# Kernel tuning notes

Measured on AMD Instinct MI355X. Metric: run time of the kernel, lower is better.

Reference implementation:

```python
import jax, jax.numpy as jnp
import numpy as np

B, L, D = 4, 4096, 1024  # batch, seq, d_model == in_features == out_features
E, R = 8, 8              # n_experts, r_base
DH = D // 2              # router hidden


def setup_inputs() -> dict:
    key = jax.random.key(0)
    ks = jax.random.split(key, 8)
    s = 0.02
    return {
        "x": jax.random.normal(ks[0], (B, L, D), dtype=jnp.float32),
        "W_base": jax.random.normal(ks[1], (D, D), dtype=jnp.float32) * s,
        "router_W1": jax.random.normal(ks[2], (DH, D), dtype=jnp.float32) * s,
        "router_b1": jnp.zeros((DH,), dtype=jnp.float32),
        "router_W2": jax.random.normal(ks[3], (E, DH), dtype=jnp.float32) * s,
        "router_b2": jnp.zeros((E,), dtype=jnp.float32),
        "temperature": jnp.asarray(1.0, dtype=jnp.float32),
        "lora_A": jax.random.normal(ks[4], (E, R, D), dtype=jnp.float32) * s,
        "lora_B": jax.random.normal(ks[5], (E, D, R), dtype=jnp.float32) * s,
    }


def reference(x, W_base, router_W1, router_b1, router_W2, router_b2,
              temperature, lora_A, lora_B):
    # Base frozen linear (bias=False): [B,L,D]
    base = jnp.einsum("bld,od->blo", x, W_base)
    # Router (eval mode: dropout inactive). hidden_states = x (Identity projection).
    h = jax.nn.relu(jnp.einsum("bld,hd->blh", x, router_W1) + router_b1)
    logits = (jnp.einsum("blh,eh->ble", h, router_W2) + router_b2) / temperature
    gates = jax.nn.softmax(logits, axis=-1)  # softmax over experts, [B,L,E]
    # All experts' low-rank projections batched: x @ A_e.T -> [B,L,E,R]
    xa = jnp.einsum("bld,erd->bler", x, lora_A)
    # Gate-weighted up-projection and sum over experts: [B,L,D]
    lora_out = jnp.einsum("bler,ble,edr->bld", xa, gates, lora_B)
    return base + lora_out
```

## Files before the change

### kernel.cpp

```cpp
#include <hip/hip_runtime.h>
#include <hip/hip_bf16.h>
#include <stdint.h>
#include <math.h>


#define M_TOK 16384

typedef unsigned short u16;
typedef short bf16x8 __attribute__((ext_vector_type(8)));
typedef float f32x4 __attribute__((ext_vector_type(4)));
typedef __attribute__((address_space(3))) uint32_t lds_u32_t;
typedef __attribute__((address_space(1))) const uint32_t glb_u32_t;

__device__ __forceinline__ u16 f2bf(float f) {
  uint32_t u = __builtin_bit_cast(uint32_t, f);
  return (u16)((u + 0x7fffu + ((u >> 16) & 1u)) >> 16);
}
__device__ __forceinline__ float bf2f(u16 v) {
  return __builtin_bit_cast(float, (uint32_t)v << 16);
}

#define VMCNT(n) asm volatile("s_waitcnt vmcnt(%0)" ::"i"(n) : "memory")
#define BAR asm volatile("s_barrier" ::: "memory")
#define SP(x) __builtin_amdgcn_s_setprio(x)

__global__ __launch_bounds__(256) void prep_k(const float* __restrict__ x,
                                              const float* __restrict__ Wb,
                                              const float* __restrict__ rW1,
                                              const float* __restrict__ rW2,
                                              const float* __restrict__ loraA,
                                              const float* __restrict__ loraB,
                                              u16* __restrict__ xb,
                                              u16* __restrict__ Btb,
                                              u16* __restrict__ W1b,
                                              u16* __restrict__ W2b,
                                              u16* __restrict__ A2b) {
  const int g = blockIdx.x;
  const int tid = threadIdx.x;
  if (g < 16384) {
    int i = g * 256 + tid;
    float4 v = ((const float4*)x)[i];
    ushort4 o;
    o.x = f2bf(v.x); o.y = f2bf(v.y); o.z = f2bf(v.z); o.w = f2bf(v.w);
    ((ushort4*)xb)[i] = o;
  } else if (g < 17408) {
    int i = (g - 16384) * 256 + tid;
    int idx = i * 4;
    int row = idx >> 10, col = idx & 1023;
    float4 v = ((const float4*)Wb)[i];
    ushort4 o;
    o.x = f2bf(v.x); o.y = f2bf(v.y); o.z = f2bf(v.z); o.w = f2bf(v.w);
    *(ushort4*)(Btb + (size_t)row * 1088 + col) = o;
  } else if (g < 17920) {
    int i = (g - 17408) * 256 + tid;
    float4 v = ((const float4*)rW1)[i];
    ushort4 o;
    o.x = f2bf(v.x); o.y = f2bf(v.y); o.z = f2bf(v.z); o.w = f2bf(v.w);
    ((ushort4*)W1b)[i] = o;
  } else if (g < 18176) {
    int idx = (g - 17920) * 256 + tid;
    int n = idx >> 6, q = idx & 63;
    int e = q >> 3, r = q & 7;
    Btb[(size_t)n * 1088 + 1024 + q] = f2bf(loraB[((size_t)(e * 1024 + n)) * 8 + r]);
  } else if (g < 18240) {
    int i = (g - 18176) * 256 + tid;
    float4 v = ((const float4*)loraA)[i];
    ushort4 o;
    o.x = f2bf(v.x); o.y = f2bf(v.y); o.z = f2bf(v.z); o.w = f2bf(v.w);
    ((ushort4*)A2b)[i] = o;
  } else {
    int i = (g - 18240) * 256 + tid;
    int idx = i * 4;
    int row = idx >> 9, col = idx & 511;
    ushort4 o = {0, 0, 0, 0};
    if (row < 8) {
      float4 v = *(const float4*)(rW2 + (size_t)row * 512 + col);
      o.x = f2bf(v.x); o.y = f2bf(v.y); o.z = f2bf(v.z); o.w = f2bf(v.w);
    }
    ((ushort4*)W2b)[i] = o;
  }
}

__global__ __launch_bounds__(256) void gemm_w(const u16* __restrict__ A,
                                              const u16* __restrict__ Bt,
                                              const float* __restrict__ part,
                                              const float* __restrict__ b2,
                                              const float* __restrict__ temp,
                                              u16* __restrict__ Cv) {
  constexpr int BM = 64, BN = 64, FM = 2, FN = 2, AI = 2, BI = 2;
  __shared__ u16 lds[(BM + BN) * 64];
  __shared__ float g_lds[64][8];
  u16* As = lds;
  u16* Bs = lds + BM * 64;

  const int tid = threadIdx.x;
  const int w = tid >> 6, lane = tid & 63;
  const int wr = w >> 1, wc = w & 1;
  const int m0 = blockIdx.y * BM;

  if (tid < 64) {
    const int m = m0 + tid;
    float lg[8] = {};
#pragma unroll
    for (int q = 0; q < 4; ++q) {
      const float4* pp = (const float4*)(part + ((size_t)q * M_TOK + m) * 8);
      float4 a = pp[0], b = pp[1];
      lg[0] += a.x; lg[1] += a.y; lg[2] += a.z; lg[3] += a.w;
      lg[4] += b.x; lg[5] += b.y; lg[6] += b.z; lg[7] += b.w;
    }
    float t = temp[0], mx = -1e30f;
#pragma unroll
    for (int e = 0; e < 8; ++e) { lg[e] = (lg[e] + b2[e]) / t; mx = fmaxf(mx, lg[e]); }
    float s = 0.f;
#pragma unroll
    for (int e = 0; e < 8; ++e) { lg[e] = expf(lg[e] - mx); s += lg[e]; }
    float inv = 1.f / s;
#pragma unroll
    for (int e = 0; e < 8; ++e) g_lds[tid][e] = lg[e] * inv;
  }

  const uint8_t* Ab = (const uint8_t*)A;
  const uint8_t* Bb = (const uint8_t*)Bt;
  f32x4 acc[FM][FN] = {};

  for (int kt = 0; kt < 16; ++kt) {
#pragma unroll
    for (int i = 0; i < AI; ++i) {
      const int lbase = (w * AI + i) * 1024;
      const int o = lbase + lane * 16;
      const int r = o >> 7, cb = o & 127;
      const uint8_t* g = Ab + (size_t)(m0 + r) * 2048 + (size_t)kt * 128 + cb;
      __builtin_amdgcn_global_load_lds((glb_u32_t*)g,
                                       (lds_u32_t*)((uint8_t*)As + lbase), 16, 0, 0);
    }
#pragma unroll
    for (int i = 0; i < BI; ++i) {
      const int lbase = (w * BI + i) * 1024;
      const int o = lbase + lane * 16;
      const int r = o >> 7, cb = o & 127;
      const uint8_t* g = Bb + (size_t)r * 2048 + (size_t)kt * 128 + cb;
      __builtin_amdgcn_global_load_lds((glb_u32_t*)g,
                                       (lds_u32_t*)((uint8_t*)Bs + lbase), 16, 0, 0);
    }
    __syncthreads();

    bf16x8 af[2][FM], bfv[2][FN];
#pragma unroll
    for (int ks = 0; ks < 2; ++ks) {
      const int col = ks * 32 + ((lane >> 4) << 3);
#pragma unroll
      for (int im = 0; im < FM; ++im) {
        const int row = wr * 32 + im * 16 + (lane & 15);
        af[ks][im] = *(const bf16x8*)(As + row * 64 + col);
      }
#pragma unroll
      for (int in_ = 0; in_ < FN; ++in_) {
        const int row = wc * 32 + in_ * 16 + (lane & 15);
        bfv[ks][in_] = *(const bf16x8*)(Bs + row * 64 + col);
      }
    }
#pragma unroll
    for (int ks = 0; ks < 2; ++ks)
#pragma unroll
      for (int im = 0; im < FM; ++im)
#pragma unroll
        for (int in_ = 0; in_ < FN; ++in_)
          acc[im][in_] = __builtin_amdgcn_mfma_f32_16x16x32_bf16(
              af[ks][im], bfv[ks][in_], acc[im][in_], 0, 0, 0);
    __syncthreads();
  }

#pragma unroll
  for (int im = 0; im < FM; ++im)
#pragma unroll
    for (int in_ = 0; in_ < FN; ++in_) {
      const int col = wc * 32 + in_ * 16 + (lane & 15);
#pragma unroll
      for (int j = 0; j < 4; ++j) {
        const int lrow = wr * 32 + im * 16 + ((lane >> 4) << 2) + j;
        float v = acc[im][in_][j] * g_lds[lrow][col >> 3];
        Cv[(size_t)(m0 + lrow) * 64 + col] = f2bf(v);
      }
    }
}

__global__ __launch_bounds__(512, 2) void gemm_h(const u16* __restrict__ A,
                                                 const u16* __restrict__ Bt,
                                                 const u16* __restrict__ W2bv,
                                                 float* __restrict__ part,
                                                 const float* __restrict__ aux,
                                                 const int N, const int K,
                                                 const int lda, const int ldb) {
  constexpr int BM = 256, BN = 128, FMH = 4;
  constexpr int BUFB = (BM + BN) * 128;

  __shared__ __align__(16) uint8_t lds[2 * BUFB];

  const int tid = threadIdx.x;
  const int lane = tid & 63, w = tid >> 6;
  const int wr = w >> 2, wcn = w & 3;
  const int l15 = lane & 15, lhi = lane >> 4;
  const int xorv = (lane & 7) << 4;
  const int c0 = (lhi * 16) ^ xorv;
  const int c1 = (64 + lhi * 16) ^ xorv;

  const int f = blockIdx.x;
  const int idx = (f & 7) * 32 + (f >> 3);
  const int gx = N / BN;
  const int m0 = (idx / gx) * BM;
  const int n0 = (idx % gx) * BN;

  const size_t lda_b = (size_t)lda * 2, ldb_b = (size_t)ldb * 2;
  const int nk = K >> 6;
  const int arow0 = (wr * (BM / 2) + l15) * 128;
  const int brow0 = (wcn * (BN / 4) + l15) * 128;

  f32x4 acc[8][2] = {};
  bf16x8 A0f[FMH][2], A1f[FMH][2];
  bf16x8 Bf[2][2];

  auto stageA = [&](int h, int kt, int b) {
    const int ktc = kt < nk ? kt : nk - 1;
    uint8_t* dst = lds + b * BUFB + h * (BM * 64) + w * 1024;
#pragma unroll
    for (int i = 0; i < 2; ++i) {
      const int off = i * 8192 + tid * 16;
      const int row = h * (BM / 2) + (off >> 7);
      const int ss = ((off >> 4) & 7) ^ (row & 7);
      const uint8_t* g =
          (const uint8_t*)A + (size_t)(m0 + row) * lda_b + ktc * 128 + ss * 16;
      __builtin_amdgcn_global_load_lds((glb_u32_t*)g, (lds_u32_t*)(dst + i * 8192),
                                       16, 0, 0);
    }
  };
  auto stageB = [&](int kt, int b) {
    const int ktc = kt < nk ? kt : nk - 1;
    uint8_t* dst = lds + b * BUFB + BM * 128 + w * 1024;
#pragma unroll
    for (int i = 0; i < 2; ++i) {
      const int off = i * 8192 + tid * 16;
      const int row = off >> 7;
      const int ss = ((off >> 4) & 7) ^ (row & 7);
      const uint8_t* g =
          (const uint8_t*)Bt + (size_t)(n0 + row) * ldb_b + ktc * 128 + ss * 16;
      __builtin_amdgcn_global_load_lds((glb_u32_t*)g, (lds_u32_t*)(dst + i * 8192),
                                       16, 0, 0);
    }
  };
  auto loadA = [&](int mh, const uint8_t* buf, bf16x8 (&dst)[FMH][2]) {
#pragma unroll
    for (int im2 = 0; im2 < FMH; ++im2) {
      const uint8_t* p = buf + arow0 + mh * (FMH * 2048) + im2 * 2048;
      dst[im2][0] = *(const bf16x8*)(p + c0);
      dst[im2][1] = *(const bf16x8*)(p + c1);
    }
  };
  auto loadB = [&](const uint8_t* buf) {
#pragma unroll
    for (int nh = 0; nh < 2; ++nh) {
      const uint8_t* p = buf + BM * 128 + brow0 + nh * 2048;
      Bf[nh][0] = *(const bf16x8*)(p + c0);
      Bf[nh][1] = *(const bf16x8*)(p + c1);
    }
  };

#define H_MFMA(mh, AF)                                                         \
  _Pragma("unroll") for (int im2 = 0; im2 < FMH; ++im2)                        \
  _Pragma("unroll") for (int nh = 0; nh < 2; ++nh)                             \
  _Pragma("unroll") for (int ks = 0; ks < 2; ++ks)                             \
      acc[(mh) * FMH + im2][nh] = __builtin_amdgcn_mfma_f32_16x16x32_bf16(     \
          AF[im2][ks], Bf[nh][ks], acc[(mh) * FMH + im2][nh], 0, 0, 0);

  stageB(0, 0);
  stageA(0, 0, 0); stageA(1, 0, 0);
  stageB(1, 1);

#pragma unroll 1
  for (int t = 0; t < nk; ++t) {
    const int p = t & 1, q = p ^ 1;
    const uint8_t* bp = (const uint8_t*)lds + p * BUFB;
    stageA(0, t + 1, q); stageA(1, t + 1, q);
    VMCNT(6);
    BAR;
    loadB(bp);
    loadA(0, bp, A0f);
    SP(1); H_MFMA(0, A0f); SP(0);
    loadA(1, bp, A1f);
    BAR;
    stageB(t + 2, p);
    BAR;
    SP(1); H_MFMA(1, A1f); SP(0);
    BAR;
  }

  u16* hs = (u16*)lds;
  __syncthreads();
#pragma unroll
  for (int im = 0; im < 8; ++im) {
#pragma unroll
    for (int in_ = 0; in_ < 2; ++in_) {
      const int col = wcn * 32 + in_ * 16 + l15;
#pragma unroll
      for (int j = 0; j < 4; ++j) {
        const int row = wr * 128 + im * 16 + lhi * 4 + j;
        float v = fmaxf(acc[im][in_][j] + aux[n0 + col], 0.f);
        hs[row * 132 + col] = f2bf(v);
      }
    }
  }
  __syncthreads();
  const u16* w2b = W2bv;
  f32x4 acc2[2] = {};
#pragma unroll
  for (int ks = 0; ks < 4; ++ks) {
    bf16x8 bfrag = *(const bf16x8*)(w2b + (size_t)l15 * 512 + n0 + ks * 32 + lhi * 8);
#pragma unroll
    for (int im2 = 0; im2 < 2; ++im2) {
      const int mrow = w * 32 + im2 * 16 + l15;
      bf16x8 afrag = *(const bf16x8*)(hs + mrow * 132 + ks * 32 + lhi * 8);
      acc2[im2] = __builtin_amdgcn_mfma_f32_16x16x32_bf16(afrag, bfrag, acc2[im2],
                                                          0, 0, 0);
    }
  }
  if (l15 < 8) {
    const size_t base = (size_t)(n0 >> 7) * M_TOK;
#pragma unroll
    for (int im2 = 0; im2 < 2; ++im2)
#pragma unroll
      for (int j = 0; j < 4; ++j) {
        const int row = m0 + w * 32 + im2 * 16 + lhi * 4 + j;
        part[(base + row) * 8 + l15] = acc2[im2][j];
      }
  }
}

#define MFMA_Q2(mh, nh, AF, BF)                                                \
  _Pragma("unroll") for (int im2 = 0; im2 < 4; ++im2)                          \
  _Pragma("unroll") for (int in2 = 0; in2 < 2; ++in2)                          \
  _Pragma("unroll") for (int ks = 0; ks < 2; ++ks)                             \
      acc[(mh) * 4 + im2][(nh) * 2 + in2] =                                    \
          __builtin_amdgcn_mfma_f32_16x16x32_bf16(                             \
              AF[im2][ks], BF[in2][ks],                                        \
              acc[(mh) * 4 + im2][(nh) * 2 + in2], 0, 0, 0);

__global__ __launch_bounds__(512, 2) void gemm_out(const u16* __restrict__ A,
                                                   const u16* __restrict__ Bt,
                                                   const u16* __restrict__ A2,
                                                   float* __restrict__ C,
                                                   const int N, const int K,
                                                   const int lda, const int ldb) {
  constexpr int BM = 256, BN = 256;
  constexpr int VMC = 4;
  constexpr int BUFB = (BM + BN) * 128;

  __shared__ __align__(16) uint8_t lds[2 * BUFB];

  const int tid = threadIdx.x;
  const int lane = tid & 63, w = tid >> 6;
  const int wr = w >> 2, wcn = w & 3;
  const int l15 = lane & 15, lhi = lane >> 4;
  const int xorv = (lane & 7) << 4;
  const int c0 = (lhi * 16) ^ xorv;
  const int c1 = (64 + lhi * 16) ^ xorv;

  const int f = blockIdx.x;
  const int idx = (f & 7) * 32 + (f >> 3);
  const int gx = N / BN;
  const int m0 = (idx / gx) * BM;
  const int n0 = (idx % gx) * BN;

  const size_t lda_b = (size_t)lda * 2, ldb_b = (size_t)ldb * 2;
  const int nk = K >> 6;
  const int arow0 = (wr * (BM / 2) + l15) * 128;
  const int brow0 = (wcn * (BN / 4) + l15) * 128;

  f32x4 acc[8][4] = {};
  bf16x8 A0f[4][2], A1f[4][2];
  bf16x8 B0f[2][2], B1f[2][2];

  auto stageA = [&](int h, int kt, int b) {
    const int ktc = kt < nk ? kt : nk - 1;
    const bool last = (ktc == nk - 1);
    uint8_t* dst = lds + b * BUFB + h * (BM * 64) + w * 1024;
#pragma unroll
    for (int i = 0; i < 2; ++i) {
      const int off = i * 8192 + tid * 16;
      const int row = h * (BM / 2) + (off >> 7);
      const int ss = ((off >> 4) & 7) ^ (row & 7);
      const uint8_t* g =
          last ? (const uint8_t*)A2 + (size_t)(m0 + row) * 128 + ss * 16
               : (const uint8_t*)A + (size_t)(m0 + row) * lda_b + ktc * 128 + ss * 16;
      __builtin_amdgcn_global_load_lds((glb_u32_t*)g, (lds_u32_t*)(dst + i * 8192),
                                       16, 0, 0);
    }
  };
  auto stageB = [&](int h, int kt, int b) {
    const int ktc = kt < nk ? kt : nk - 1;
    uint8_t* dst = lds + b * BUFB + BM * 128 + h * (BN * 64) + w * 1024;
#pragma unroll
    for (int i = 0; i < 2; ++i) {
      const int off = i * 8192 + tid * 16;
      const int row = h * (BN / 2) + (off >> 7);
      const int ss = ((off >> 4) & 7) ^ (row & 7);
      const uint8_t* g =
          (const uint8_t*)Bt + (size_t)(n0 + row) * ldb_b + ktc * 128 + ss * 16;
      __builtin_amdgcn_global_load_lds((glb_u32_t*)g, (lds_u32_t*)(dst + i * 8192),
                                       16, 0, 0);
    }
  };
  auto loadA = [&](int mh, const uint8_t* buf, bf16x8 (&dst)[4][2]) {
#pragma unroll
    for (int im2 = 0; im2 < 4; ++im2) {
      const uint8_t* p = buf + arow0 + mh * (4 * 2048) + im2 * 2048;
      dst[im2][0] = *(const bf16x8*)(p + c0);
      dst[im2][1] = *(const bf16x8*)(p + c1);
    }
  };
  auto loadB = [&](int nh, const uint8_t* buf, bf16x8 (&dst)[2][2]) {
#pragma unroll
    for (int in2 = 0; in2 < 2; ++in2) {
      const uint8_t* p = buf + BM * 128 + brow0 + nh * (2 * 2048) + in2 * 2048;
      dst[in2][0] = *(const bf16x8*)(p + c0);
      dst[in2][1] = *(const bf16x8*)(p + c1);
    }
  };

  const uint8_t* b0 = lds;
  const uint8_t* b1 = lds + BUFB;

  stageA(0, 0, 0); stageA(1, 0, 0);
  stageB(0, 0, 0); stageB(1, 0, 0);
  stageB(0, 1, 1); stageB(1, 1, 1);
  VMCNT(VMC); BAR;
  loadA(0, b0, A0f); loadB(0, b0, B0f);

  const int NIT = nk >> 1;
#pragma unroll 1
  for (int it = 0; it < NIT; ++it) {
    const int t = it * 2;
    stageA(0, t + 1, 1);
    BAR;
    SP(1); MFMA_Q2(0, 0, A0f, B0f); SP(0);
    loadB(1, b0, B1f);
    BAR;
    stageA(1, t + 1, 1);
    BAR;
    SP(1); MFMA_Q2(0, 1, A0f, B1f); SP(0);
    loadA(1, b0, A1f);
    BAR;
    stageB(0, t + 2, 0);
    BAR;
    SP(1); MFMA_Q2(1, 1, A1f, B1f); SP(0);
    BAR;
    stageB(1, t + 2, 0);
    VMCNT(VMC);
    BAR;
    SP(1); MFMA_Q2(1, 0, A1f, B0f); SP(0);
    loadA(0, b1, A0f); loadB(0, b1, B0f);
    BAR;
    stageA(0, t + 2, 0);
    BAR;
    SP(1); MFMA_Q2(0, 0, A0f, B0f); SP(0);
    loadB(1, b1, B1f);
    BAR;
    stageA(1, t + 2, 0);
    BAR;
    SP(1); MFMA_Q2(0, 1, A0f, B1f); SP(0);
    loadA(1, b1, A1f);
    BAR;
    stageB(0, t + 3, 1);
    BAR;
    SP(1); MFMA_Q2(1, 1, A1f, B1f); SP(0);
    BAR;
    stageB(1, t + 3, 1);
    VMCNT(VMC);
    BAR;
    SP(1); MFMA_Q2(1, 0, A1f, B0f); SP(0);
    loadA(0, b0, A0f); loadB(0, b0, B0f);
    BAR;
  }

  if (nk & 1) {
    SP(1); MFMA_Q2(0, 0, A0f, B0f); SP(0);
    loadB(1, b0, B1f);
    SP(1); MFMA_Q2(0, 1, A0f, B1f); SP(0);
    loadA(1, b0, A1f);
    SP(1); MFMA_Q2(1, 1, A1f, B1f); MFMA_Q2(1, 0, A1f, B0f); SP(0);
  }

#pragma unroll
  for (int im = 0; im < 8; ++im) {
#pragma unroll
    for (int in_ = 0; in_ < 4; ++in_) {
      const int col = n0 + wcn * 64 + in_ * 16 + l15;
#pragma unroll
      for (int j = 0; j < 4; ++j) {
        const int row = m0 + wr * 128 + im * 16 + lhi * 4 + j;
        C[(size_t)row * N + col] = acc[im][in_][j];
      }
    }
  }
}

extern "C" void kernel_launch(void* const* d_in, const int* in_sizes, int n_in,
                              void* d_out, int out_size, void* d_ws, size_t ws_size,
                              hipStream_t stream) {
  const float* x     = (const float*)d_in[0];
  const float* Wb    = (const float*)d_in[1];
  const float* rW1   = (const float*)d_in[2];
  const float* rb1   = (const float*)d_in[3];
  const float* rW2   = (const float*)d_in[4];
  const float* rb2   = (const float*)d_in[5];
  const float* temp  = (const float*)d_in[6];
  const float* loraA = (const float*)d_in[7];
  const float* loraB = (const float*)d_in[8];
  float* out = (float*)d_out;

  uint8_t* p = (uint8_t*)d_ws;
  u16* xb    = (u16*)p;   p += (size_t)M_TOK * 1024 * 2;
  u16* wb    = (u16*)p;   p += (size_t)M_TOK * 64 * 2;
  u16* Btb   = (u16*)p;   p += (size_t)1024 * 1088 * 2;
  u16* W1b   = (u16*)p;   p += (size_t)512 * 1024 * 2;
  u16* W2b   = (u16*)p;   p += (size_t)16 * 512 * 2;
  u16* A2b   = (u16*)p;   p += (size_t)64 * 1024 * 2;
  float* part = (float*)p;

  prep_k<<<18248, 256, 0, stream>>>(x, Wb, rW1, rW2, loraA, loraB,
                                    xb, Btb, W1b, W2b, A2b);

  gemm_h<<<256, 512, 0, stream>>>(xb, W1b, W2b, part, rb1, 512, 1024, 1024, 1024);

  gemm_w<<<dim3(1, M_TOK / 64), 256, 0, stream>>>(xb, A2b, part, rb2, temp, wb);

  gemm_out<<<256, 512, 0, stream>>>(xb, Btb, wb, out, 1024, 1088, 1024, 1088);
}
```

Before: 94.51 us.

## Fuse x bf16 conversion and router softmax into restructured router GEMM

```diff
diff --git a/kernel.cpp b/kernel.cpp
--- a/kernel.cpp
+++ b/kernel.cpp
@@ -16,60 +16,56 @@
   uint32_t u = __builtin_bit_cast(uint32_t, f);
   return (u16)((u + 0x7fffu + ((u >> 16) & 1u)) >> 16);
 }
-__device__ __forceinline__ float bf2f(u16 v) {
-  return __builtin_bit_cast(float, (uint32_t)v << 16);
+__device__ __forceinline__ int cvtpk(float lo, float hi) {
+  int r;
+  asm("v_cvt_pk_bf16_f32 %0, %1, %2" : "=v"(r) : "v"(lo), "v"(hi));
+  return r;
 }
 
 #define VMCNT(n) asm volatile("s_waitcnt vmcnt(%0)" ::"i"(n) : "memory")
+#define LGKM0 asm volatile("s_waitcnt lgkmcnt(0)" ::: "memory")
 #define BAR asm volatile("s_barrier" ::: "memory")
+#define MEMFENCE asm volatile("" ::: "memory")
 #define SP(x) __builtin_amdgcn_s_setprio(x)
 
-__global__ __launch_bounds__(256) void prep_k(const float* __restrict__ x,
-                                              const float* __restrict__ Wb,
+__global__ __launch_bounds__(256) void prep_k(const float* __restrict__ Wb,
                                               const float* __restrict__ rW1,
                                               const float* __restrict__ rW2,
                                               const float* __restrict__ loraA,
                                               const float* __restrict__ loraB,
-                                              u16* __restrict__ xb,
                                               u16* __restrict__ Btb,
                                               u16* __restrict__ W1b,
                                               u16* __restrict__ W2b,
                                               u16* __restrict__ A2b) {
   const int g = blockIdx.x;
   const int tid = threadIdx.x;
-  if (g < 16384) {
+  if (g < 1024) {
     int i = g * 256 + tid;
-    float4 v = ((const float4*)x)[i];
-    ushort4 o;
-    o.x = f2bf(v.x); o.y = f2bf(v.y); o.z = f2bf(v.z); o.w = f2bf(v.w);
-    ((ushort4*)xb)[i] = o;
-  } else if (g < 17408) {
-    int i = (g - 16384) * 256 + tid;
     int idx = i * 4;
     int row = idx >> 10, col = idx & 1023;
     float4 v = ((const float4*)Wb)[i];
     ushort4 o;
     o.x = f2bf(v.x); o.y = f2bf(v.y); o.z = f2bf(v.z); o.w = f2bf(v.w);
     *(ushort4*)(Btb + (size_t)row * 1088 + col) = o;
-  } else if (g < 17920) {
-    int i = (g - 17408) * 256 + tid;
+  } else if (g < 1536) {
+    int i = (g - 1024) * 256 + tid;
     float4 v = ((const float4*)rW1)[i];
     ushort4 o;
     o.x = f2bf(v.x); o.y = f2bf(v.y); o.z = f2bf(v.z); o.w = f2bf(v.w);
     ((ushort4*)W1b)[i] = o;
-  } else if (g < 18176) {
-    int idx = (g - 17920) * 256 + tid;
+  } else if (g < 1792) {
+    int idx = (g - 1536) * 256 + tid;
     int n = idx >> 6, q = idx & 63;
     int e = q >> 3, r = q & 7;
     Btb[(size_t)n * 1088 + 1024 + q] = f2bf(loraB[((size_t)(e * 1024 + n)) * 8 + r]);
-  } else if (g < 18240) {
-    int i = (g - 18176) * 256 + tid;
+  } else if (g < 1856) {
+    int i = (g - 1792) * 256 + tid;
     float4 v = ((const float4*)loraA)[i];
     ushort4 o;
     o.x = f2bf(v.x); o.y = f2bf(v.y); o.z = f2bf(v.z); o.w = f2bf(v.w);
     ((ushort4*)A2b)[i] = o;
   } else {
-    int i = (g - 18240) * 256 + tid;
+    int i = (g - 1856) * 256 + tid;
     int idx = i * 4;
     int row = idx >> 9, col = idx & 511;
     ushort4 o = {0, 0, 0, 0};
@@ -81,11 +77,183 @@
   }
 }
 
+__global__ __launch_bounds__(512, 2) void gemm_h(const float* __restrict__ x,
+                                                 const u16* __restrict__ W1b,
+                                                 const u16* __restrict__ W2bv,
+                                                 u16* __restrict__ xb,
+                                                 float* __restrict__ gates,
+                                                 const float* __restrict__ b1,
+                                                 const float* __restrict__ b2,
+                                                 const float* __restrict__ temp,
+                                                 const int K) {
+  constexpr int ABUF = 64 * 128;
+  constexpr int BBUF = 512 * 128;
+  constexpr int BUFB = ABUF + BBUF;
+  __shared__ __align__(16) uint8_t lds[2 * BUFB];
+
+  const int tid = threadIdx.x;
+  const int lane = tid & 63, w = tid >> 6;
+  const int l15 = lane & 15, lhi = lane >> 4;
+  const int xorv = (lane & 7) << 4;
+  const int c0 = (lhi * 16) ^ xorv;
+  const int c1 = (64 + lhi * 16) ^ xorv;
+
+  const int f = blockIdx.x;
+  const int m0 = ((f & 7) * 32 + (f >> 3)) * 64;
+
+  const int nk = K >> 6;
+  const int xrow = tid >> 3, xsub = tid & 7;
+
+  f32x4 acc[4][4] = {};
+  bf16x8 af[4][2], bfv[4][2];
+  float4 xA0, xA1, xB0, xB1;
+
+  auto stageBH = [&](int kt, int b) {
+    const int ktc = kt < nk ? kt : nk - 1;
+    uint8_t* dst = lds + b * BUFB + ABUF + w * 1024;
+#pragma unroll
+    for (int i = 0; i < 8; ++i) {
+      const int off = i * 8192 + tid * 16;
+      const int row = off >> 7;
+      const int ss = ((off >> 4) & 7) ^ (row & 7);
+      const uint8_t* g =
+          (const uint8_t*)W1b + (size_t)row * 2048 + ktc * 128 + ss * 16;
+      __builtin_amdgcn_global_load_lds((glb_u32_t*)g, (lds_u32_t*)(dst + i * 8192),
+                                       16, 0, 0);
+    }
+  };
+  auto issueX = [&](int kt, float4& ra, float4& rb) {
+    const int ktc = kt < nk ? kt : nk - 1;
+    const float* gp = x + (size_t)(m0 + xrow) * 1024 + ktc * 64 + xsub * 8;
+    ra = *(const float4*)gp;
+    rb = *(const float4*)(gp + 4);
+  };
+  auto writeA = [&](int kt, int b, const float4& ra, const float4& rb) {
+    const int ktc = kt < nk ? kt : nk - 1;
+    int4 sv;
+    sv.x = cvtpk(ra.x, ra.y); sv.y = cvtpk(ra.z, ra.w);
+    sv.z = cvtpk(rb.x, rb.y); sv.w = cvtpk(rb.z, rb.w);
+    *(int4*)(lds + b * BUFB + xrow * 128 + ((xsub ^ (xrow & 7)) << 4)) = sv;
+    *(int4*)(xb + (size_t)(m0 + xrow) * 1024 + ktc * 64 + xsub * 8) = sv;
+  };
+  auto loadAH = [&](const uint8_t* bufA) {
+#pragma unroll
+    for (int mf = 0; mf < 4; ++mf) {
+      const uint8_t* pr = bufA + (mf * 16 + l15) * 128;
+      af[mf][0] = *(const bf16x8*)(pr + c0);
+      af[mf][1] = *(const bf16x8*)(pr + c1);
+    }
+  };
+  auto loadBH = [&](const uint8_t* bufB) {
+#pragma unroll
+    for (int nf = 0; nf < 4; ++nf) {
+      const uint8_t* pr = bufB + (w * 64 + nf * 16 + l15) * 128;
+      bfv[nf][0] = *(const bf16x8*)(pr + c0);
+      bfv[nf][1] = *(const bf16x8*)(pr + c1);
+    }
+  };
+
+#define HMM()                                                                  \
+  _Pragma("unroll") for (int mf = 0; mf < 4; ++mf)                             \
+  _Pragma("unroll") for (int nf = 0; nf < 4; ++nf)                             \
+  _Pragma("unroll") for (int ks = 0; ks < 2; ++ks)                             \
+      acc[mf][nf] = __builtin_amdgcn_mfma_f32_16x16x32_bf16(                   \
+          af[mf][ks], bfv[nf][ks], acc[mf][nf], 0, 0, 0);
+
+  {
+    const float* gp = x + (size_t)(m0 + xrow) * 1024 + xsub * 8;
+    float4 a = *(const float4*)gp, b = *(const float4*)(gp + 4);
+    int4 sv;
+    sv.x = cvtpk(a.x, a.y); sv.y = cvtpk(a.z, a.w);
+    sv.z = cvtpk(b.x, b.y); sv.w = cvtpk(b.z, b.w);
+    *(int4*)(lds + xrow * 128 + ((xsub ^ (xrow & 7)) << 4)) = sv;
+    *(int4*)(xb + (size_t)(m0 + xrow) * 1024 + xsub * 8) = sv;
+  }
+  stageBH(0, 0);
+  MEMFENCE;
+  issueX(1, xA0, xA1);
+  VMCNT(2);
+  LGKM0;
+  BAR;
+
+  const int nit = nk >> 1;
+#pragma unroll 1
+  for (int it = 0; it < nit; ++it) {
+    const int t = it * 2;
+    loadAH(lds);
+    loadBH(lds + ABUF);
+    stageBH(t + 1, 1);
+    MEMFENCE;
+    issueX(t + 2, xB0, xB1);
+    MEMFENCE;
+    VMCNT(10);
+    writeA(t + 1, 1, xA0, xA1);
+    SP(1); HMM(); SP(0);
+    LGKM0; VMCNT(3); BAR;
+    loadAH(lds + BUFB);
+    loadBH(lds + BUFB + ABUF);
+    stageBH(t + 2, 0);
+    MEMFENCE;
+    issueX(t + 3, xA0, xA1);
+    MEMFENCE;
+    VMCNT(10);
+    writeA(t + 2, 0, xB0, xB1);
+    SP(1); HMM(); SP(0);
+    LGKM0; VMCNT(3); BAR;
+  }
+
+  u16* hs = (u16*)lds;
+  __syncthreads();
+#pragma unroll
+  for (int mf = 0; mf < 4; ++mf) {
+#pragma unroll
+    for (int nf = 0; nf < 4; ++nf) {
+      const int col = w * 64 + nf * 16 + l15;
+#pragma unroll
+      for (int j = 0; j < 4; ++j) {
+        const int row = mf * 16 + lhi * 4 + j;
+        float v = fmaxf(acc[mf][nf][j] + b1[col], 0.f);
+        hs[row * 520 + col] = f2bf(v);
+      }
+    }
+  }
+  __syncthreads();
+  if (w < 4) {
+    f32x4 acc2 = {};
+#pragma unroll
+    for (int ks = 0; ks < 16; ++ks) {
+      bf16x8 bfrag = *(const bf16x8*)(W2bv + (size_t)l15 * 512 + ks * 32 + lhi * 8);
+      bf16x8 afrag = *(const bf16x8*)(hs + (w * 16 + l15) * 520 + ks * 32 + lhi * 8);
+      acc2 = __builtin_amdgcn_mfma_f32_16x16x32_bf16(afrag, bfrag, acc2, 0, 0, 0);
+    }
+    if (l15 < 8) {
+      float t = temp[0];
+      float lg[4];
+#pragma unroll
+      for (int j = 0; j < 4; ++j) lg[j] = (acc2[j] + b2[l15]) / t;
+      float mx[4], sm[4];
+#pragma unroll
+      for (int j = 0; j < 4; ++j) mx[j] = lg[j];
+#pragma unroll
+      for (int m = 1; m <= 4; m <<= 1)
+#pragma unroll
+        for (int j = 0; j < 4; ++j) mx[j] = fmaxf(mx[j], __shfl_xor(mx[j], m));
+#pragma unroll
+      for (int j = 0; j < 4; ++j) { lg[j] = expf(lg[j] - mx[j]); sm[j] = lg[j]; }
+#pragma unroll
+      for (int m = 1; m <= 4; m <<= 1)
+#pragma unroll
+        for (int j = 0; j < 4; ++j) sm[j] += __shfl_xor(sm[j], m);
+#pragma unroll
+      for (int j = 0; j < 4; ++j)
+        gates[(size_t)(m0 + w * 16 + lhi * 4 + j) * 8 + l15] = lg[j] / sm[j];
+    }
+  }
+}
+
 __global__ __launch_bounds__(256) void gemm_w(const u16* __restrict__ A,
                                               const u16* __restrict__ Bt,
-                                              const float* __restrict__ part,
-                                              const float* __restrict__ b2,
-                                              const float* __restrict__ temp,
+                                              const float* __restrict__ gates,
                                               u16* __restrict__ Cv) {
   constexpr int BM = 64, BN = 64, FM = 2, FN = 2, AI = 2, BI = 2;
   __shared__ u16 lds[(BM + BN) * 64];
@@ -99,24 +267,10 @@
   const int m0 = blockIdx.y * BM;
 
   if (tid < 64) {
-    const int m = m0 + tid;
-    float lg[8] = {};
-#pragma unroll
-    for (int q = 0; q < 4; ++q) {
-      const float4* pp = (const float4*)(part + ((size_t)q * M_TOK + m) * 8);
-      float4 a = pp[0], b = pp[1];
-      lg[0] += a.x; lg[1] += a.y; lg[2] += a.z; lg[3] += a.w;
-      lg[4] += b.x; lg[5] += b.y; lg[6] += b.z; lg[7] += b.w;
-    }
-    float t = temp[0], mx = -1e30f;
-#pragma unroll
-    for (int e = 0; e < 8; ++e) { lg[e] = (lg[e] + b2[e]) / t; mx = fmaxf(mx, lg[e]); }
-    float s = 0.f;
-#pragma unroll
-    for (int e = 0; e < 8; ++e) { lg[e] = expf(lg[e] - mx); s += lg[e]; }
-    float inv = 1.f / s;
-#pragma unroll
-    for (int e = 0; e < 8; ++e) g_lds[tid][e] = lg[e] * inv;
+    const float4* gp = (const float4*)(gates + (size_t)(m0 + tid) * 8);
+    float4 a = gp[0], b = gp[1];
+    g_lds[tid][0] = a.x; g_lds[tid][1] = a.y; g_lds[tid][2] = a.z; g_lds[tid][3] = a.w;
+    g_lds[tid][4] = b.x; g_lds[tid][5] = b.y; g_lds[tid][6] = b.z; g_lds[tid][7] = b.w;
   }
 
   const uint8_t* Ab = (const uint8_t*)A;
@@ -182,156 +336,6 @@
         Cv[(size_t)(m0 + lrow) * 64 + col] = f2bf(v);
       }
     }
-}
-
-__global__ __launch_bounds__(512, 2) void gemm_h(const u16* __restrict__ A,
-                                                 const u16* __restrict__ Bt,
-                                                 const u16* __restrict__ W2bv,
-                                                 float* __restrict__ part,
-                                                 const float* __restrict__ aux,
-                                                 const int N, const int K,
-                                                 const int lda, const int ldb) {
-  constexpr int BM = 256, BN = 128, FMH = 4;
-  constexpr int BUFB = (BM + BN) * 128;
-
-  __shared__ __align__(16) uint8_t lds[2 * BUFB];
-
-  const int tid = threadIdx.x;
-  const int lane = tid & 63, w = tid >> 6;
-  const int wr = w >> 2, wcn = w & 3;
-  const int l15 = lane & 15, lhi = lane >> 4;
-  const int xorv = (lane & 7) << 4;
-  const int c0 = (lhi * 16) ^ xorv;
-  const int c1 = (64 + lhi * 16) ^ xorv;
-
-  const int f = blockIdx.x;
-  const int idx = (f & 7) * 32 + (f >> 3);
-  const int gx = N / BN;
-  const int m0 = (idx / gx) * BM;
-  const int n0 = (idx % gx) * BN;
-
-  const size_t lda_b = (size_t)lda * 2, ldb_b = (size_t)ldb * 2;
-  const int nk = K >> 6;
-  const int arow0 = (wr * (BM / 2) + l15) * 128;
-  const int brow0 = (wcn * (BN / 4) + l15) * 128;
-
-  f32x4 acc[8][2] = {};
-  bf16x8 A0f[FMH][2], A1f[FMH][2];
-  bf16x8 Bf[2][2];
-
-  auto stageA = [&](int h, int kt, int b) {
-    const int ktc = kt < nk ? kt : nk - 1;
-    uint8_t* dst = lds + b * BUFB + h * (BM * 64) + w * 1024;
-#pragma unroll
-    for (int i = 0; i < 2; ++i) {
-      const int off = i * 8192 + tid * 16;
-      const int row = h * (BM / 2) + (off >> 7);
-      const int ss = ((off >> 4) & 7) ^ (row & 7);
-      const uint8_t* g =
-          (const uint8_t*)A + (size_t)(m0 + row) * lda_b + ktc * 128 + ss * 16;
-      __builtin_amdgcn_global_load_lds((glb_u32_t*)g, (lds_u32_t*)(dst + i * 8192),
-                                       16, 0, 0);
-    }
-  };
-  auto stageB = [&](int kt, int b) {
-    const int ktc = kt < nk ? kt : nk - 1;
-    uint8_t* dst = lds + b * BUFB + BM * 128 + w * 1024;
-#pragma unroll
-    for (int i = 0; i < 2; ++i) {
-      const int off = i * 8192 + tid * 16;
-      const int row = off >> 7;
-      const int ss = ((off >> 4) & 7) ^ (row & 7);
-      const uint8_t* g =
-          (const uint8_t*)Bt + (size_t)(n0 + row) * ldb_b + ktc * 128 + ss * 16;
-      __builtin_amdgcn_global_load_lds((glb_u32_t*)g, (lds_u32_t*)(dst + i * 8192),
-                                       16, 0, 0);
-    }
-  };
-  auto loadA = [&](int mh, const uint8_t* buf, bf16x8 (&dst)[FMH][2]) {
-#pragma unroll
-    for (int im2 = 0; im2 < FMH; ++im2) {
-      const uint8_t* p = buf + arow0 + mh * (FMH * 2048) + im2 * 2048;
-      dst[im2][0] = *(const bf16x8*)(p + c0);
-      dst[im2][1] = *(const bf16x8*)(p + c1);
-    }
-  };
-  auto loadB = [&](const uint8_t* buf) {
-#pragma unroll
-    for (int nh = 0; nh < 2; ++nh) {
-      const uint8_t* p = buf + BM * 128 + brow0 + nh * 2048;
-      Bf[nh][0] = *(const bf16x8*)(p + c0);
-      Bf[nh][1] = *(const bf16x8*)(p + c1);
-    }
-  };
-
-#define H_MFMA(mh, AF)                                                         \
-  _Pragma("unroll") for (int im2 = 0; im2 < FMH; ++im2)                        \
-  _Pragma("unroll") for (int nh = 0; nh < 2; ++nh)                             \
-  _Pragma("unroll") for (int ks = 0; ks < 2; ++ks)                             \
-      acc[(mh) * FMH + im2][nh] = __builtin_amdgcn_mfma_f32_16x16x32_bf16(     \
-          AF[im2][ks], Bf[nh][ks], acc[(mh) * FMH + im2][nh], 0, 0, 0);
-
-  stageB(0, 0);
-  stageA(0, 0, 0); stageA(1, 0, 0);
-  stageB(1, 1);
-
-#pragma unroll 1
-  for (int t = 0; t < nk; ++t) {
-    const int p = t & 1, q = p ^ 1;
-    const uint8_t* bp = (const uint8_t*)lds + p * BUFB;
-    stageA(0, t + 1, q); stageA(1, t + 1, q);
-    VMCNT(6);
-    BAR;
-    loadB(bp);
-    loadA(0, bp, A0f);
-    SP(1); H_MFMA(0, A0f); SP(0);
-    loadA(1, bp, A1f);
-    BAR;
-    stageB(t + 2, p);
-    BAR;
-    SP(1); H_MFMA(1, A1f); SP(0);
-    BAR;
-  }
-
-  u16* hs = (u16*)lds;
-  __syncthreads();
-#pragma unroll
-  for (int im = 0; im < 8; ++im) {
-#pragma unroll
-    for (int in_ = 0; in_ < 2; ++in_) {
-      const int col = wcn * 32 + in_ * 16 + l15;
-#pragma unroll
-      for (int j = 0; j < 4; ++j) {
-        const int row = wr * 128 + im * 16 + lhi * 4 + j;
-        float v = fmaxf(acc[im][in_][j] + aux[n0 + col], 0.f);
-        hs[row * 132 + col] = f2bf(v);
-      }
-    }
-  }
-  __syncthreads();
-  const u16* w2b = W2bv;
-  f32x4 acc2[2] = {};
-#pragma unroll
-  for (int ks = 0; ks < 4; ++ks) {
-    bf16x8 bfrag = *(const bf16x8*)(w2b + (size_t)l15 * 512 + n0 + ks * 32 + lhi * 8);
-#pragma unroll
-    for (int im2 = 0; im2 < 2; ++im2) {
-      const int mrow = w * 32 + im2 * 16 + l15;
-      bf16x8 afrag = *(const bf16x8*)(hs + mrow * 132 + ks * 32 + lhi * 8);
-      acc2[im2] = __builtin_amdgcn_mfma_f32_16x16x32_bf16(afrag, bfrag, acc2[im2],
-                                                          0, 0, 0);
-    }
-  }
-  if (l15 < 8) {
-    const size_t base = (size_t)(n0 >> 7) * M_TOK;
-#pragma unroll
-    for (int im2 = 0; im2 < 2; ++im2)
-#pragma unroll
-      for (int j = 0; j < 4; ++j) {
-        const int row = m0 + w * 32 + im2 * 16 + lhi * 4 + j;
-        part[(base + row) * 8 + l15] = acc2[im2][j];
-      }
-  }
 }
 
 #define MFMA_Q2(mh, nh, AF, BF)                                                \
@@ -523,14 +527,13 @@
   u16* W1b   = (u16*)p;   p += (size_t)512 * 1024 * 2;
   u16* W2b   = (u16*)p;   p += (size_t)16 * 512 * 2;
   u16* A2b   = (u16*)p;   p += (size_t)64 * 1024 * 2;
-  float* part = (float*)p;
-
-  prep_k<<<18248, 256, 0, stream>>>(x, Wb, rW1, rW2, loraA, loraB,
-                                    xb, Btb, W1b, W2b, A2b);
-
-  gemm_h<<<256, 512, 0, stream>>>(xb, W1b, W2b, part, rb1, 512, 1024, 1024, 1024);
-
-  gemm_w<<<dim3(1, M_TOK / 64), 256, 0, stream>>>(xb, A2b, part, rb2, temp, wb);
+  float* gates = (float*)p;
+
+  prep_k<<<1864, 256, 0, stream>>>(Wb, rW1, rW2, loraA, loraB, Btb, W1b, W2b, A2b);
+
+  gemm_h<<<256, 512, 0, stream>>>(x, W1b, W2b, xb, gates, rb1, rb2, temp, 1024);
+
+  gemm_w<<<dim3(1, M_TOK / 64), 256, 0, stream>>>(xb, A2b, gates, wb);
 
   gemm_out<<<256, 512, 0, stream>>>(xb, Btb, wb, out, 1024, 1088, 1024, 1088);
 }
```

Measured after the change: 92.59 us. 1.02x faster.
